# Kernel tuning notes

Measured on AMD Instinct MI355X. Metric: run time of the kernel, lower is better.

Reference implementation:

```python
import jax, jax.numpy as jnp
import numpy as np

D_Z = 1024
D_MODEL = 4096
EPS = 1e-5  # torch LayerNorm default
CLAMP = 3.0


def setup_inputs() -> dict:
    key = jax.random.key(0)
    k_z, k_w, k_b = jax.random.split(key, 3)
    z = jax.random.normal(k_z, (8, 2048, D_Z), dtype=jnp.float32)
    # LayerNorm params (gamma=1, beta=0 init in torch; keep learnable form)
    ln_gamma = jnp.ones((D_Z,), dtype=jnp.float32)
    ln_beta = jnp.zeros((D_Z,), dtype=jnp.float32)
    # Linear: torch default init U(-1/sqrt(d_z), 1/sqrt(d_z))
    bound = 1.0 / np.sqrt(D_Z)
    W = jax.random.uniform(k_w, (D_Z, D_MODEL), minval=-bound, maxval=bound, dtype=jnp.float32)
    b = jax.random.uniform(k_b, (D_MODEL,), minval=-bound, maxval=bound, dtype=jnp.float32)
    scale = jnp.ones((1,), dtype=jnp.float32)
    return {"z": z, "ln_gamma": ln_gamma, "ln_beta": ln_beta, "W": W, "b": b, "scale": scale}


def reference(z, ln_gamma, ln_beta, W, b, scale):
    # LayerNorm over last dim
    mu = jnp.mean(z, axis=-1, keepdims=True)
    var = jnp.mean(jnp.square(z - mu), axis=-1, keepdims=True)
    zn = (z - mu) * jax.lax.rsqrt(var + EPS) * ln_gamma + ln_beta
    # Linear -> scalar scale -> tanh clamp
    x = (jnp.einsum('bsd,dm->bsm', zn, W) + b) * scale
    return jnp.tanh(x / CLAMP) * CLAMP
```

## Files before the change

kernel.cpp:

```cpp
#include <hip/hip_runtime.h>

#define M_DIM 16384
#define K_DIM 1024
#define N_DIM 4096

typedef __bf16 bf16x8 __attribute__((ext_vector_type(8)));
typedef float f32x4 __attribute__((ext_vector_type(4)));

__device__ __forceinline__ unsigned short f2bf(float f) {
    union { float f; unsigned int i; } v; v.f = f;
    unsigned int r = v.i + 0x7fffu + ((v.i >> 16) & 1u);
    return (unsigned short)(r >> 16);
}
__device__ __forceinline__ unsigned int pack2(float lo, float hi) {
    return ((unsigned int)f2bf(lo)) | (((unsigned int)f2bf(hi)) << 16);
}

__global__ __launch_bounds__(256) void ln_kernel(
        const float* __restrict__ z,
        const float* __restrict__ gamma,
        const float* __restrict__ beta,
        unsigned short* __restrict__ zn) {
    const int wave = threadIdx.x >> 6;
    const int lane = threadIdx.x & 63;
    const size_t row = (size_t)blockIdx.x * 4 + wave;
    const float* zr = z + row * K_DIM + lane * 16;

    float x[16];
#pragma unroll
    for (int v = 0; v < 4; v++) {
        float4 p = ((const float4*)zr)[v];
        x[v * 4 + 0] = p.x; x[v * 4 + 1] = p.y; x[v * 4 + 2] = p.z; x[v * 4 + 3] = p.w;
    }

    float s = 0.f, ss = 0.f;
#pragma unroll
    for (int i = 0; i < 16; i++) { s += x[i]; ss += x[i] * x[i]; }
#pragma unroll
    for (int o = 32; o; o >>= 1) { s += __shfl_xor(s, o, 64); ss += __shfl_xor(ss, o, 64); }
    const float mean = s * (1.f / K_DIM);
    const float var = ss * (1.f / K_DIM) - mean * mean;
    const float rstd = rsqrtf(var + 1e-5f);

    float gv[16], bv[16];
    const float* gp = gamma + lane * 16;
    const float* bp = beta + lane * 16;
#pragma unroll
    for (int v = 0; v < 4; v++) {
        float4 g = ((const float4*)gp)[v];
        float4 b = ((const float4*)bp)[v];
        gv[v * 4 + 0] = g.x; gv[v * 4 + 1] = g.y; gv[v * 4 + 2] = g.z; gv[v * 4 + 3] = g.w;
        bv[v * 4 + 0] = b.x; bv[v * 4 + 1] = b.y; bv[v * 4 + 2] = b.z; bv[v * 4 + 3] = b.w;
    }

    float o16[16];
#pragma unroll
    for (int i = 0; i < 16; i++) o16[i] = (x[i] - mean) * rstd * gv[i] + bv[i];

    uint4 q0, q1;
    q0.x = pack2(o16[0], o16[1]);  q0.y = pack2(o16[2], o16[3]);
    q0.z = pack2(o16[4], o16[5]);  q0.w = pack2(o16[6], o16[7]);
    q1.x = pack2(o16[8], o16[9]);  q1.y = pack2(o16[10], o16[11]);
    q1.z = pack2(o16[12], o16[13]); q1.w = pack2(o16[14], o16[15]);
    unsigned short* zo = zn + row * K_DIM + lane * 16;
    *(uint4*)(zo) = q0;
    *(uint4*)(zo + 8) = q1;
}

__global__ __launch_bounds__(256) void tr_kernel(
        const float* __restrict__ W, unsigned short* __restrict__ Wt) {
    __shared__ float t[32][33];
    const int tx = threadIdx.x, ty = threadIdx.y;
    const int n0 = blockIdx.x * 32, k0 = blockIdx.y * 32;
#pragma unroll
    for (int j = 0; j < 32; j += 8)
        t[ty + j][tx] = W[(size_t)(k0 + ty + j) * N_DIM + n0 + tx];
    __syncthreads();
#pragma unroll
    for (int j = 0; j < 32; j += 8)
        Wt[(size_t)(n0 + ty + j) * K_DIM + k0 + tx] = f2bf(t[tx][ty + j]);
}

__device__ __forceinline__ void async_copy16(const unsigned short* g, unsigned short* l) {
    __builtin_amdgcn_global_load_lds(
        (const __attribute__((address_space(1))) unsigned int*)g,
        (__attribute__((address_space(3))) unsigned int*)l,
        16, 0, 0);
}

__global__ __launch_bounds__(256) void gemm_kernel(
        const unsigned short* __restrict__ A,
        const unsigned short* __restrict__ B,
        const float* __restrict__ bias,
        const float* __restrict__ scale,
        float* __restrict__ out) {
    __shared__ __align__(16) unsigned short As[128 * 32];
    __shared__ __align__(16) unsigned short Bs[128 * 32];

    const int tid = threadIdx.x;
    const int wave = tid >> 6, lane = tid & 63;
    const int wm = wave >> 1, wn = wave & 1;
    const int bn = blockIdx.x, bm = blockIdx.y;
    const int l15 = lane & 15, l4 = lane >> 4;

    const int sr = lane >> 2;
    const int sc = (lane & 3) * 8;
    const unsigned short* ag0 = A + (size_t)(bm * 128 + wave * 32 + sr) * K_DIM + sc;
    const unsigned short* bg0 = B + (size_t)(bn * 128 + wave * 32 + sr) * K_DIM + sc;
    unsigned short* as0 = &As[wave * 1024];
    unsigned short* bs0 = &Bs[wave * 1024];

    f32x4 acc[4][4] = {};

    for (int k0 = 0; k0 < K_DIM; k0 += 32) {
        __syncthreads();
        async_copy16(ag0 + k0, as0);
        async_copy16(ag0 + k0 + 16 * K_DIM, as0 + 512);
        async_copy16(bg0 + k0, bs0);
        async_copy16(bg0 + k0 + 16 * K_DIM, bs0 + 512);
        __syncthreads();

        bf16x8 a[4], b[4];
#pragma unroll
        for (int i = 0; i < 4; i++)
            a[i] = *(const bf16x8*)&As[(wm * 64 + i * 16 + l15) * 32 + l4 * 8];
#pragma unroll
        for (int i = 0; i < 4; i++)
            b[i] = *(const bf16x8*)&Bs[(wn * 64 + i * 16 + l15) * 32 + l4 * 8];
#pragma unroll
        for (int i = 0; i < 4; i++)
#pragma unroll
            for (int j = 0; j < 4; j++)
                acc[i][j] = __builtin_amdgcn_mfma_f32_16x16x32_bf16(a[i], b[j], acc[i][j], 0, 0, 0);
    }

    const float scl = scale[0];
#pragma unroll
    for (int j = 0; j < 4; j++) {
        const int gcol = bn * 128 + wn * 64 + j * 16 + l15;
        const float bv = bias[gcol];
#pragma unroll
        for (int i = 0; i < 4; i++) {
            const int grow = bm * 128 + wm * 64 + i * 16 + l4 * 4;
#pragma unroll
            for (int r = 0; r < 4; r++) {
                float x = (acc[i][j][r] + bv) * scl;
                float y = x * (1.0f / 3.0f);
                y = fminf(fmaxf(y, -15.f), 15.f);
                const float e = __expf(2.f * y);
                out[(size_t)(grow + r) * N_DIM + gcol] = 3.f * (e - 1.f) / (e + 1.f);
            }
        }
    }
}

extern "C" void kernel_launch(void* const* d_in, const int* in_sizes, int n_in,
                              void* d_out, int out_size, void* d_ws, size_t ws_size,
                              hipStream_t stream) {
    const float* z     = (const float*)d_in[0];
    const float* gamma = (const float*)d_in[1];
    const float* beta  = (const float*)d_in[2];
    const float* W     = (const float*)d_in[3];
    const float* b     = (const float*)d_in[4];
    const float* scale = (const float*)d_in[5];
    float* out = (float*)d_out;

    unsigned short* zn = (unsigned short*)d_ws;
    unsigned short* Wt = zn + (size_t)M_DIM * K_DIM;

    ln_kernel<<<M_DIM / 4, 256, 0, stream>>>(z, gamma, beta, zn);
    tr_kernel<<<dim3(N_DIM / 32, K_DIM / 32), dim3(32, 8), 0, stream>>>(W, Wt);
    gemm_kernel<<<dim3(N_DIM / 128, M_DIM / 128), 256, 0, stream>>>(zn, Wt, b, scale, out);
}
```

Baseline: 495.7 us.

## Switch GEMM to 32x32x16 MFMA with swizzled LDS and cheaper tanh epilogue

The GEMM moves from 16x16x32 MFMAs to 32x32x16 MFMAs with a 2x2 accumulator tile per wave. The LDS staging layout is XOR-swizzled at the global-to-LDS copy and at the fragment reads to cut bank conflicts. The tanh epilogue is rewritten as exp2 plus a hardware reciprocal, with the 2/3·log2(e) factor folded into one multiplier. The LayerNorm kernel switches to an interleaved float4 access pattern for coalescing. Risks are small accuracy changes from the approximate rcp and the removed exponent clamp, and correctness of the new swizzle mapping.

```diff
diff --git a/kernel.cpp b/kernel.cpp
--- a/kernel.cpp
+++ b/kernel.cpp
@@ -5,7 +5,7 @@
 #define N_DIM 4096
 
 typedef __bf16 bf16x8 __attribute__((ext_vector_type(8)));
-typedef float f32x4 __attribute__((ext_vector_type(4)));
+typedef float f32x16 __attribute__((ext_vector_type(16)));
 
 __device__ __forceinline__ unsigned short f2bf(float f) {
     union { float f; unsigned int i; } v; v.f = f;
@@ -24,47 +24,35 @@
     const int wave = threadIdx.x >> 6;
     const int lane = threadIdx.x & 63;
     const size_t row = (size_t)blockIdx.x * 4 + wave;
-    const float* zr = z + row * K_DIM + lane * 16;
+    const float* zr = z + row * K_DIM;
 
-    float x[16];
+    float4 x[4];
 #pragma unroll
-    for (int v = 0; v < 4; v++) {
-        float4 p = ((const float4*)zr)[v];
-        x[v * 4 + 0] = p.x; x[v * 4 + 1] = p.y; x[v * 4 + 2] = p.z; x[v * 4 + 3] = p.w;
-    }
+    for (int v = 0; v < 4; v++) x[v] = *(const float4*)(zr + v * 256 + lane * 4);
 
     float s = 0.f, ss = 0.f;
 #pragma unroll
-    for (int i = 0; i < 16; i++) { s += x[i]; ss += x[i] * x[i]; }
+    for (int v = 0; v < 4; v++) {
+        s  += x[v].x + x[v].y + x[v].z + x[v].w;
+        ss += x[v].x * x[v].x + x[v].y * x[v].y + x[v].z * x[v].z + x[v].w * x[v].w;
+    }
 #pragma unroll
     for (int o = 32; o; o >>= 1) { s += __shfl_xor(s, o, 64); ss += __shfl_xor(ss, o, 64); }
     const float mean = s * (1.f / K_DIM);
     const float var = ss * (1.f / K_DIM) - mean * mean;
     const float rstd = rsqrtf(var + 1e-5f);
 
-    float gv[16], bv[16];
-    const float* gp = gamma + lane * 16;
-    const float* bp = beta + lane * 16;
 #pragma unroll
     for (int v = 0; v < 4; v++) {
-        float4 g = ((const float4*)gp)[v];
-        float4 b = ((const float4*)bp)[v];
-        gv[v * 4 + 0] = g.x; gv[v * 4 + 1] = g.y; gv[v * 4 + 2] = g.z; gv[v * 4 + 3] = g.w;
-        bv[v * 4 + 0] = b.x; bv[v * 4 + 1] = b.y; bv[v * 4 + 2] = b.z; bv[v * 4 + 3] = b.w;
+        float4 g = *(const float4*)(gamma + v * 256 + lane * 4);
+        float4 b = *(const float4*)(beta + v * 256 + lane * 4);
+        float o0 = (x[v].x - mean) * rstd * g.x + b.x;
+        float o1 = (x[v].y - mean) * rstd * g.y + b.y;
+        float o2 = (x[v].z - mean) * rstd * g.z + b.z;
+        float o3 = (x[v].w - mean) * rstd * g.w + b.w;
+        uint2 q; q.x = pack2(o0, o1); q.y = pack2(o2, o3);
+        *(uint2*)(zn + row * K_DIM + v * 256 + lane * 4) = q;
     }
-
-    float o16[16];
-#pragma unroll
-    for (int i = 0; i < 16; i++) o16[i] = (x[i] - mean) * rstd * gv[i] + bv[i];
-
-    uint4 q0, q1;
-    q0.x = pack2(o16[0], o16[1]);  q0.y = pack2(o16[2], o16[3]);
-    q0.z = pack2(o16[4], o16[5]);  q0.w = pack2(o16[6], o16[7]);
-    q1.x = pack2(o16[8], o16[9]);  q1.y = pack2(o16[10], o16[11]);
-    q1.z = pack2(o16[12], o16[13]); q1.w = pack2(o16[14], o16[15]);
-    unsigned short* zo = zn + row * K_DIM + lane * 16;
-    *(uint4*)(zo) = q0;
-    *(uint4*)(zo + 8) = q1;
 }
 
 __global__ __launch_bounds__(256) void tr_kernel(
@@ -101,16 +89,18 @@
     const int wave = tid >> 6, lane = tid & 63;
     const int wm = wave >> 1, wn = wave & 1;
     const int bn = blockIdx.x, bm = blockIdx.y;
-    const int l15 = lane & 15, l4 = lane >> 4;
+    const int l31 = lane & 31, lhi = lane >> 5;
 
     const int sr = lane >> 2;
-    const int sc = (lane & 3) * 8;
+    const int sc = ((lane & 3) ^ ((lane >> 3) & 3)) * 8;
     const unsigned short* ag0 = A + (size_t)(bm * 128 + wave * 32 + sr) * K_DIM + sc;
     const unsigned short* bg0 = B + (size_t)(bn * 128 + wave * 32 + sr) * K_DIM + sc;
     unsigned short* as0 = &As[wave * 1024];
     unsigned short* bs0 = &Bs[wave * 1024];
 
-    f32x4 acc[4][4] = {};
+    f32x16 acc[2][2] = {};
+
+    const int swz = (l31 >> 1) & 3;
 
     for (int k0 = 0; k0 < K_DIM; k0 += 32) {
         __syncthreads();
@@ -120,35 +110,38 @@
         async_copy16(bg0 + k0 + 16 * K_DIM, bs0 + 512);
         __syncthreads();
 
-        bf16x8 a[4], b[4];
 #pragma unroll
-        for (int i = 0; i < 4; i++)
-            a[i] = *(const bf16x8*)&As[(wm * 64 + i * 16 + l15) * 32 + l4 * 8];
+        for (int s = 0; s < 2; s++) {
+            const int c = s * 2 + lhi;
+            bf16x8 a[2], b[2];
 #pragma unroll
-        for (int i = 0; i < 4; i++)
-            b[i] = *(const bf16x8*)&Bs[(wn * 64 + i * 16 + l15) * 32 + l4 * 8];
+            for (int i = 0; i < 2; i++)
+                a[i] = *(const bf16x8*)&As[(wm * 64 + i * 32 + l31) * 32 + (c ^ swz) * 8];
 #pragma unroll
-        for (int i = 0; i < 4; i++)
+            for (int j = 0; j < 2; j++)
+                b[j] = *(const bf16x8*)&Bs[(wn * 64 + j * 32 + l31) * 32 + (c ^ swz) * 8];
 #pragma unroll
-            for (int j = 0; j < 4; j++)
-                acc[i][j] = __builtin_amdgcn_mfma_f32_16x16x32_bf16(a[i], b[j], acc[i][j], 0, 0, 0);
+            for (int i = 0; i < 2; i++)
+#pragma unroll
+                for (int j = 0; j < 2; j++)
+                    acc[i][j] = __builtin_amdgcn_mfma_f32_32x32x16_bf16(a[i], b[j], acc[i][j], 0, 0, 0);
+        }
     }
 
-    const float scl = scale[0];
+    const float mfac = scale[0] * 0.96179669392236f;
 #pragma unroll
-    for (int j = 0; j < 4; j++) {
-        const int gcol = bn * 128 + wn * 64 + j * 16 + l15;
+    for (int j = 0; j < 2; j++) {
+        const int gcol = bn * 128 + wn * 64 + j * 32 + l31;
         const float bv = bias[gcol];
 #pragma unroll
-        for (int i = 0; i < 4; i++) {
-            const int grow = bm * 128 + wm * 64 + i * 16 + l4 * 4;
+        for (int i = 0; i < 2; i++) {
+            const int rbase = bm * 128 + wm * 64 + i * 32 + 4 * lhi;
 #pragma unroll
-            for (int r = 0; r < 4; r++) {
-                float x = (acc[i][j][r] + bv) * scl;
-                float y = x * (1.0f / 3.0f);
-                y = fminf(fmaxf(y, -15.f), 15.f);
-                const float e = __expf(2.f * y);
-                out[(size_t)(grow + r) * N_DIM + gcol] = 3.f * (e - 1.f) / (e + 1.f);
+            for (int r = 0; r < 16; r++) {
+                const int grow = rbase + (r & 3) + 8 * (r >> 2);
+                float t = (acc[i][j][r] + bv) * mfac;
+                float e = __builtin_amdgcn_exp2f(t);
+                out[(size_t)grow * N_DIM + gcol] = 3.f - 6.f * __builtin_amdgcn_rcpf(e + 1.f);
             }
         }
     }
```

Measured after the change: 484.4 us. 2.3% less time.
